# Kernel optimization log

Measured on AMD Instinct MI355X. Metric: run time of the kernel, lower is better.

Reference implementation:

```python
import jax, jax.numpy as jnp
import numpy as np

H = W = 256
L = H * W                      # number of graph vertices / tree leaves
N_NODES = 2 * L - 1            # binary partition tree node count
LAM = 1.0                      # lambda_ (soft-area temperature)


def _grid_edges():
    """4-adjacency grid graph edges (same structure as higra get_4_adjacency_graph)."""
    idx = np.arange(L, dtype=np.int64).reshape(H, W)
    src = np.concatenate([idx[:, :-1].ravel(), idx[:-1, :].ravel()])
    dst = np.concatenate([idx[:, 1:].ravel(), idx[1:, :].ravel()])
    return src.astype(np.int32), dst.astype(np.int32)


def setup_inputs() -> dict:
    key = jax.random.key(0)
    src, dst = _grid_edges()
    ew = jax.random.uniform(key, (src.shape[0],), dtype=jnp.float32)
    return {"edge_weights": ew,
            "edges_src": jnp.asarray(src),
            "edges_dst": jnp.asarray(dst)}


def _build_tree(ew, src, dst):
    """higra.bpt_canonical: Kruskal over stably-sorted edges, building a binary
    merge tree. Leaves are 0..L-1, internal node L+i is created by the i-th MST
    edge. Returns (sizes, mst_edge_map, ancestor paths). All integer structure
    is piecewise-constant w.r.t. edge_weights (no gradient flows through it)."""
    order = np.argsort(ew, kind="stable")
    uf = np.arange(L)

    def find(x):
        r = x
        while uf[r] != r:
            r = uf[r]
        while uf[x] != r:
            uf[x], x = r, uf[x]
        return r

    canon = np.arange(L)                      # tree node of each union-find root
    parent = np.arange(N_NODES)               # self-parent until set (root keeps self)
    sizes = np.ones(N_NODES, dtype=np.float32)
    edge_map = np.zeros(L - 1, dtype=np.int64)
    node = L
    for ei in order:
        a = find(src[ei]); b = find(dst[ei])
        if a == b:
            continue
        na, nb = canon[a], canon[b]
        parent[na] = node
        parent[nb] = node
        sizes[node] = sizes[na] + sizes[nb]
        edge_map[node - L] = ei
        uf[a] = b
        canon[b] = node
        node += 1
    # self-inclusive ancestor paths, padded by repeating the root
    cur = np.arange(N_NODES)
    cols = [cur.copy()]
    while np.any(parent[cur] != cur):
        cur = parent[cur]
        cols.append(cur.copy())
    paths = np.stack(cols, axis=1)            # [N_NODES, D+1]
    return sizes, edge_map, paths


def _softarea(edge_weights, edge_map, sizes_np, paths_np):
    """Soft area of every tree node n:
       area(n) = sum_x sigmoid((alt(n) - d(x, n)) / lambda)
    where d(x,n) is the min ultrametric distance from leaf x to the leaves of n:
      - x in subtree(n), x != n : d = alt(parent(x))
      - x == n (leaf)           : d = 0
      - x outside subtree(n)    : d = alt(lowest ancestor of n containing x).
    Outside leaves are grouped per ancestor a (count = size(a) - size(previous
    node on the path)), giving an O(N * depth) vectorized computation."""
    alt = jnp.concatenate([jnp.zeros((L,), edge_weights.dtype),
                           edge_weights[edge_map]])          # [N_NODES]
    alt_path = alt[paths_np]                                  # [N, D+1]
    size_path = sizes_np[paths_np]                            # constant, numpy
    diff = jnp.asarray(size_path[:, 1:] - size_path[:, :-1])  # 0 on root padding
    outside = jnp.sum(
        diff * jax.nn.sigmoid((alt[:, None] - alt_path[:, 1:]) / LAM), axis=1)

    # inside: each leaf x contributes sigmoid((alt(a_k) - alt(parent(x)))/lam)
    # to every proper ancestor a_k, plus sigmoid(0)=0.5 to itself (alt(leaf)=0).
    lp = paths_np[:L]                                         # [L, D+1]
    alt_lp = alt_path[:L]
    valid = jnp.asarray((lp[:, 1:] != lp[:, :-1]).astype(np.float32))
    vals = jax.nn.sigmoid((alt_lp[:, 1:] - alt_lp[:, 1:2]) / LAM) * valid
    inside = jax.ops.segment_sum(vals.reshape(-1),
                                 jnp.asarray(lp[:, 1:].reshape(-1)),
                                 num_segments=N_NODES)
    inside = inside.at[:L].add(0.5)
    return inside + outside


def reference(edge_weights, edges_src, edges_dst):
    sizes, edge_map, paths = _build_tree(np.asarray(edge_weights),
                                         np.asarray(edges_src),
                                         np.asarray(edges_dst))
    return _softarea(edge_weights, jnp.asarray(edge_map), sizes, paths)
```

## Files before the change

### kernel.cpp

```cpp
#include <hip/hip_runtime.h>
#include <stdint.h>

typedef unsigned int u32;
typedef unsigned short u16;

#define L_VERTS 65536
#define N_EDGES 130560
#define N_NODES 131071
#define NODEPAD 131072

#define CCH 170
#define SCH 768
#define MAXSV 1536
#define HSZ 2048

#define NB 255
#define TPB 64
#define IPT 8
#define IPB 512

__global__ void init_keys(const float* __restrict__ w, u32* __restrict__ keys, u32* __restrict__ vals){
  int i = blockIdx.x*blockDim.x + threadIdx.x;
  if(i < N_EDGES){ keys[i] = __float_as_uint(w[i]); vals[i] = (u32)i; }
}

__global__ void radix_hist(const u32* __restrict__ idx, const u32* __restrict__ keys,
                           u32* __restrict__ histG, int shift){
  __shared__ u32 h[256];
  for(int i=threadIdx.x;i<256;i+=TPB) h[i]=0;
  __syncthreads();
  int base = blockIdx.x*IPB + threadIdx.x*IPT;
  #pragma unroll
  for(int i=0;i<IPT;i++){
    u32 e = idx[base+i];
    u32 d = (keys[e]>>shift)&255u;
    atomicAdd(&h[d],1u);
  }
  __syncthreads();
  for(int i=threadIdx.x;i<256;i+=TPB) histG[i*NB+blockIdx.x]=h[i];
}

__global__ void radix_scan(u32* histG){
  const int M = 256*NB;
  __shared__ u32 sums[1024];
  int t=threadIdx.x; int s=t*64; u32 acc=0;
  for(int i=0;i<64;i++){int id=s+i; if(id<M) acc+=histG[id];}
  sums[t]=acc; __syncthreads();
  for(int off=1; off<1024; off<<=1){
    u32 v=(t>=off)?sums[t-off]:0u;
    __syncthreads();
    sums[t]+=v;
    __syncthreads();
  }
  u32 run = (t==0)?0u:sums[t-1];
  for(int i=0;i<64;i++){int id=s+i; if(id<M){u32 v=histG[id]; histG[id]=run; run+=v;}}
}

__global__ void radix_scatter(const u32* __restrict__ idxIn, const u32* __restrict__ keys,
                              u32* __restrict__ idxOut, const u32* __restrict__ histG, int shift){
  __shared__ u16 thoff[256][TPB];
  int t=threadIdx.x;
  for(int d=t;d<256;d+=TPB) for(int j=0;j<TPB;j++) thoff[d][j]=0;
  __syncthreads();
  int base = blockIdx.x*IPB + t*IPT;
  u32 myv[IPT]; u32 myd[IPT];
  #pragma unroll
  for(int i=0;i<IPT;i++){
    myv[i]=idxIn[base+i];
    myd[i]=(keys[myv[i]]>>shift)&255u;
    thoff[myd[i]][t]++;
  }
  __syncthreads();
  for(int dd=0;dd<4;dd++){
    int d=t*4+dd; u32 run=0;
    for(int j=0;j<TPB;j++){ u32 v=thoff[d][j]; thoff[d][j]=(u16)run; run+=v; }
  }
  __syncthreads();
  #pragma unroll
  for(int i=0;i<IPT;i++){
    u32 d=myd[i];
    u32 pos = histG[d*NB+blockIdx.x] + (u32)thoff[d][t];
    thoff[d][t]++;
    idxOut[pos]=myv[i];
  }
}

__global__ void build_epair(const u32* __restrict__ order, const int* __restrict__ srcv,
                            const int* __restrict__ dstv, u32* __restrict__ epair){
  int p=blockIdx.x*blockDim.x+threadIdx.x;
  if(p>=N_EDGES) return;
  u32 e=order[p];
  epair[p]=((u32)dstv[e]<<16)|(u32)srcv[e];
}

__global__ void init_all(u32* szG,u16* canonTop16,u32* parent,float* alt){
  int i=blockIdx.x*blockDim.x+threadIdx.x;
  if(i<N_NODES){ parent[i]=(u32)i; alt[i]=0.f; }
  if(i<L_VERTS){ szG[i]=1u; canonTop16[i]=0xFFFFu; }
}

__device__ __forceinline__ u32 ald(u32* p){
  return __hip_atomic_load(p, __ATOMIC_RELAXED, __HIP_MEMORY_SCOPE_AGENT);
}
__device__ __forceinline__ void ast(u32* p, u32 v){
  __hip_atomic_store(p, v, __ATOMIC_RELAXED, __HIP_MEMORY_SCOPE_AGENT);
}

__global__ void __launch_bounds__(1024,1) p1_checkpoints(
    const u32* __restrict__ epair,
    u32* szG, u16* lid16, u16* svroot16, u16* svsize16, u16* svnext16, u32* mG)
{
  __shared__ u16 ufL[L_VERTS];
  __shared__ u32 hkey[HSZ];
  __shared__ u32 sufL[MAXSV];
  __shared__ u32 compsz[MAXSV];
  __shared__ u32 repkey[MAXSV];
  __shared__ u32 mcnt;
  u16* hval=(u16*)repkey;
  int t = threadIdx.x;
  for(int i=t;i<L_VERTS/2;i+=1024) ((u32*)ufL)[i]=((2u*(u32)i+1u)<<16)|(2u*(u32)i);
  for(int k=0;k<CCH;k++){
    for(int i=t;i<HSZ;i+=1024) hkey[i]=0xFFFFFFFFu;
    if(t==0) mcnt=0u;
    __syncthreads();
    int base = k*SCH;
    int myslot[2]; int mycnt=0;
    for(int i=t;i<2*SCH;i+=1024){
      u32 pr = epair[base+(i>>1)];
      u32 v = (i&1)? (pr>>16) : (pr&0xFFFFu);
      u32 x=v;
      while(true){ u32 px=ufL[x]; if(px==x)break; u32 g=ufL[px]; if(g!=px) ufL[x]=(u16)g; x=g; }
      u32 r=x;
      if(v!=r) ufL[v]=(u16)r;
      u32 h=(r*2654435761u)>>21;
      int slot;
      while(true){
        u32 old=atomicCAS(&hkey[h],0xFFFFFFFFu,r);
        if(old==0xFFFFFFFFu){
          slot=(int)h;
          u32 id=atomicAdd(&mcnt,1u);
          hval[h]=(u16)id;
          u32 sz=ald(&szG[r]);
          svroot16[k*MAXSV+id]=(u16)r;
          svsize16[k*MAXSV+id]=(u16)(sz-1u);
          break;
        }
        if(old==r){slot=(int)h;break;}
        h=(h+1)&(HSZ-1u);
      }
      myslot[mycnt++]=slot;
    }
    __syncthreads();
    {
      int c=0;
      for(int i=t;i<2*SCH;i+=1024){ lid16[2*base+i]=hval[myslot[c]]; c++; }
    }
    u32 mc=mcnt;
    if(t==0) mG[k]=mc;
    __syncthreads();
    for(u32 s=t;s<mc;s+=1024){ sufL[s]=s; compsz[s]=0u; repkey[s]=0u; }
    __syncthreads();
    for(int i=t;i<SCH;i+=1024){
      u32 lw=((u32*)lid16)[base+i];
      u32 sa=lw&0xFFFFu, sb=lw>>16;
      if(sa==sb) continue;
      while(true){
        u32 x=sa; while(true){u32 p2=sufL[x]; if(p2==x)break; u32 g=sufL[p2]; if(g!=p2) sufL[x]=g; x=g;}
        u32 y=sb; while(true){u32 p2=sufL[y]; if(p2==y)break; u32 g=sufL[p2]; if(g!=p2) sufL[y]=g; y=g;}
        if(x==y) break;
        u32 hi=x>y?x:y, lo=x^y^hi;
        if(atomicCAS(&sufL[hi],hi,lo)==hi) break;
        sa=hi; sb=lo;
      }
    }
    __syncthreads();
    for(u32 s=t;s<mc;s+=1024){
      u32 x=s; while(true){u32 p2=sufL[x]; if(p2==x)break; x=p2;}
      sufL[s]=x;
      u32 sz=(u32)svsize16[k*MAXSV+s]+1u;
      atomicAdd(&compsz[x], sz);
      atomicMax(&repkey[x], (sz<<11) | (2047u-s));
    }
    __syncthreads();
    for(u32 s=t;s<mc;s+=1024){
      u32 rs=sufL[s];
      u32 rep=2047u-(repkey[rs]&2047u);
      u32 wv=(u32)svroot16[k*MAXSV+rep];
      svnext16[k*MAXSV+s]=(u16)wv;
      u32 myroot=(u32)svroot16[k*MAXSV+s];
      if(myroot!=wv) ufL[myroot]=(u16)wv;
      if(s==rep)     ast(&szG[wv], compsz[rs]);
    }
    __syncthreads();
  }
}

__global__ void __launch_bounds__(64) p2_chunk(
  const u16* __restrict__ lid16,
  const u16* __restrict__ svsize16, const u16* __restrict__ svnext16, const u32* __restrict__ mG,
  u16* __restrict__ outChA, u16* __restrict__ outChB, u16* __restrict__ outSize16, u16* __restrict__ outJ16,
  u32* __restrict__ accCnt, u16* __restrict__ compR16, u16* __restrict__ compTop16, u32* __restrict__ ncomp)
{
  int k = blockIdx.x; int t = threadIdx.x;
  __shared__ u16 uf[MAXSV];
  __shared__ u32 csize[MAXSV];
  __shared__ u16 ctop[MAXSV];
  __shared__ u16 svnl[MAXSV];
  __shared__ u32 cmp_s;
  u32 m = mG[k];
  for(u32 s=t;s<m;s+=64){
    uf[s]=(u16)s;
    csize[s]=(u32)svsize16[k*MAXSV+s]+1u;
    ctop[s]=(u16)s;
    svnl[s]=svnext16[k*MAXSV+s];
  }
  if(t==0) cmp_s=0u;
  __syncthreads();
  if(t==0){
    int base=k*SCH;
    u32 cnt=0;
    for(int j=0;j<SCH;j++){
      u32 lw = ((const u32*)lid16)[base+j];
      u32 la = lw & 0xFFFFu, lb = lw >> 16;
      u32 x=la; while(true){u32 px=uf[x]; if(px==x)break; u32 g=uf[px]; uf[x]=(u16)g; x=g;}
      u32 y=lb; while(true){u32 py=uf[y]; if(py==y)break; u32 g=uf[py]; uf[y]=(u16)g; y=g;}
      if(x==y) continue;
      u32 sa=csize[x], sb=csize[y], ns=sa+sb;
      outChA[base+cnt]=ctop[x];
      outChB[base+cnt]=ctop[y];
      outSize16[base+cnt]=(u16)(ns-1u);
      outJ16[base+cnt]=(u16)j;
      u32 win=(sa>=sb)?x:y, los=x^y^win;
      uf[los]=(u16)win; csize[win]=ns; ctop[win]=(u16)(0x8000u|cnt);
      cnt++;
    }
    accCnt[k]=cnt;
  }
  __syncthreads();
  for(u32 s=t;s<m;s+=64){
    if(uf[s]==(u16)s && (ctop[s]&0x8000u)){
      u32 pos=atomicAdd(&cmp_s,1u);
      compR16[k*MAXSV+pos]=svnl[s];
      compTop16[k*MAXSV+pos]=(u16)(ctop[s]&0x7FFFu);
    }
  }
  __syncthreads();
  if(t==0) ncomp[k]=cmp_s;
}

__global__ void __launch_bounds__(1024) p3_stitch(
  const u32* __restrict__ accCnt, const u16* __restrict__ outChA, const u16* __restrict__ outChB,
  const u16* __restrict__ outSize16, const u16* __restrict__ outJ16,
  const u16* __restrict__ svroot16,
  const u16* __restrict__ compR16, const u16* __restrict__ compTop16, const u32* __restrict__ ncomp,
  const u32* __restrict__ order, const float* __restrict__ w,
  u16* __restrict__ canonTop16, u32* __restrict__ parent, float* __restrict__ alt, u16* __restrict__ usize16,
  u32* __restrict__ diag)
{
  __shared__ u32 accBase[CCH];
  int t=threadIdx.x;
  if(t==0){ u32 r=0; for(int k=0;k<CCH;k++){ accBase[k]=r; r+=accCnt[k]; } diag[1]=r; }
  __syncthreads();
  for(int idx=t; idx<N_EDGES; idx+=1024){
    int k = idx/SCH; int j = idx - k*SCH;
    if(j < (int)accCnt[k]){
      u32 nid = (u32)L_VERTS + accBase[k] + (u32)j;
      u32 p = (u32)(k*SCH) + (u32)outJ16[idx];
      alt[nid] = w[order[p]];
      usize16[nid] = outSize16[idx];
      u32 cA=outChA[idx]; if(cA & 0x8000u) parent[(u32)L_VERTS+accBase[k]+(cA&0x7FFFu)] = nid;
      u32 cB=outChB[idx]; if(cB & 0x8000u) parent[(u32)L_VERTS+accBase[k]+(cB&0x7FFFu)] = nid;
    }
  }
  __syncthreads();
  for(int k=0;k<CCH;k++){
    u32 ac=accCnt[k];
    for(u32 j=t;j<ac;j+=1024){
      u32 idx=(u32)(k*SCH)+j;
      u32 nid=(u32)L_VERTS+accBase[k]+j;
      u32 cA=outChA[idx];
      if(!(cA&0x8000u)){
        u32 root=(u32)svroot16[k*MAXSV+cA];
        u32 ct=(u32)canonTop16[root];
        parent[(ct==0xFFFFu)?root:((u32)L_VERTS+ct)]=nid;
      }
      u32 cB=outChB[idx];
      if(!(cB&0x8000u)){
        u32 root=(u32)svroot16[k*MAXSV+cB];
        u32 ct=(u32)canonTop16[root];
        parent[(ct==0xFFFFu)?root:((u32)L_VERTS+ct)]=nid;
      }
    }
    __syncthreads();
    u32 nc=ncomp[k];
    for(u32 j=t;j<nc;j+=1024){
      canonTop16[(u32)compR16[k*MAXSV+j]] = (u16)(accBase[k]+compTop16[k*MAXSV+j]);
    }
    __syncthreads();
  }
}

__global__ void verify_zero(u32* chsum, u32* diag){
  int i=blockIdx.x*blockDim.x+threadIdx.x;
  if(i<L_VERTS) chsum[i]=0u;
  if(i==0){ diag[0]=0u; diag[2]=0u; }
}
__global__ void verify_pass1(const u32* __restrict__ parent, const float* __restrict__ alt,
                             const u16* __restrict__ usize16, u32* chsum, u32* diag){
  int i=blockIdx.x*blockDim.x+threadIdx.x;
  if(i>=N_NODES) return;
  u32 p=parent[i];
  if(p==(u32)i){ atomicAdd(&diag[2],1u); return; }
  u32 sz = (i<L_VERTS)?1u:((u32)usize16[i]+1u);
  atomicAdd(&chsum[p-L_VERTS], sz + (1u<<24));
  if(alt[p] < alt[i]) atomicOr(&diag[0], 4u);
}
__global__ void verify_pass2(const u16* __restrict__ usize16, u32* chsum, u32* diag){
  int i=blockIdx.x*blockDim.x+threadIdx.x;
  if(i==0){
    if(diag[1]!=(u32)(L_VERTS-1)) atomicOr(&diag[0],1u);
    if(diag[2]!=1u)               atomicOr(&diag[0],2u);
  }
  if(i<L_VERTS-1){
    u32 n=(u32)L_VERTS+(u32)i;
    u32 expect=((u32)usize16[n]+1u)+(2u<<24);
    if(chsum[i]!=expect) atomicOr(&diag[0],8u);
  }
  if(i<L_VERTS) chsum[i]=0u;
}
__global__ void fixup(const u32* diag, float* out){
  u32 f=diag[0];
  if(f==0u) return;
  float v = (f&1u)?2.0e6f : (f&2u)?3.0e6f : (f&4u)?4.0e6f : 5.0e6f;
  int i=blockIdx.x*blockDim.x+threadIdx.x;
  if(i<N_NODES) out[i]=v;
}

__device__ __forceinline__ void hvals3(float v, int j0, float* o){
  float v2=v*v, v3=v2*v, v4=v2*v2, v5=v4*v;
  if(j0==0){
    o[0]=0.5f-0.25f*v+v3*(1.f/48.f)-v5*(1.f/480.f);
    o[1]=0.25f-v2*(1.f/16.f)+v4*(1.f/96.f);
    o[2]=v*(1.f/16.f)-v3*(1.f/48.f);
  }else{
    o[0]=v2*(1.f/48.f)-(1.f/48.f);
    o[1]=-v*(1.f/96.f);
    o[2]=(1.f/480.f);
  }
}

__global__ void prep_init(const u32* __restrict__ parent, const u16* __restrict__ usize16,
                          u32* cc, u32* J0, uint2* A0, float* out){
  int n=blockIdx.x*blockDim.x+threadIdx.x;
  if(n>=N_NODES) return;
  out[n] = (n<L_VERTS)?0.5f:0.0f;
  if(n==N_NODES-1){ J0[n]=(u32)n; A0[n]=make_uint2(0u,0u); return; }
  u32 p=parent[n];
  u32 ord=atomicAdd(&cc[p-L_VERTS],1u);
  u32 szP=(u32)usize16[p]+1u;
  u32 szN=(n<L_VERTS)?1u:((u32)usize16[n]+1u);
  u32 sib=szP-szN;
  A0[n]=make_uint2(ord? sib:0u, 1u + (ord? (2u*sib-1u):0u));
  J0[n]=p;
}

__global__ void double_round2(const u32* __restrict__ Jin, const uint2* __restrict__ Ain,
                              u32* __restrict__ Jout, uint2* __restrict__ Aout){
  int n=blockIdx.x*blockDim.x+threadIdx.x;
  if(n>=N_NODES) return;
  u32 j=Jin[n];
  u32 j2=Jin[j];
  u32 j3=Jin[j2];
  uint2 a=Ain[n], aj=Ain[j], b=Ain[j2], bj=Ain[j3];
  Aout[n]=make_uint2(a.x+aj.x+b.x+bj.x, a.y+aj.y+b.y+bj.y);
  Jout[n]=Jin[j3];
}

__global__ void zero_nodeM(float* nodeM){
  int i=blockIdx.x*blockDim.x+threadIdx.x;
  if(i<3*NODEPAD) nodeM[i]=0.f;
}

__global__ void leaf_scatter(const u32* __restrict__ parent, const float* __restrict__ alt,
                             const uint2* __restrict__ accF, float* __restrict__ leafM, int j0){
  int x=blockIdx.x*blockDim.x+threadIdx.x;
  if(x>=L_VERTS) return;
  float b=alt[parent[x]];
  float h[3]; hvals3(b,j0,h);
  u32 pos=accF[x].x;
  leafM[0*L_VERTS+pos]=h[0];
  leafM[1*L_VERTS+pos]=h[1];
  leafM[2*L_VERTS+pos]=h[2];
}

__global__ void node_scatter(const u32* __restrict__ parent, const float* __restrict__ alt,
                             const u16* __restrict__ usize16, const uint2* __restrict__ accF,
                             float* __restrict__ nodeM, int j0){
  int n=blockIdx.x*blockDim.x+threadIdx.x;
  if(n>=N_NODES-1) return;
  u32 p=parent[n];
  u32 szP=(u32)usize16[p]+1u;
  u32 szN=(n<L_VERTS)?1u:((u32)usize16[n]+1u);
  float d=(float)(szP-szN);
  float h[3]; hvals3(alt[p],j0,h);
  u32 q0=accF[n].y;
  u32 q1=q0 + 2u*szN - 1u;
  #pragma unroll
  for(int j=0;j<3;j++){
    float tm=d*h[j];
    atomicAdd(&nodeM[j*NODEPAD+q0], tm);
    atomicAdd(&nodeM[j*NODEPAD+q1], -tm);
  }
}

__global__ void scanA(float* M, u32 slen, float* bsum){
  int j=blockIdx.y; int b=blockIdx.x; int t=threadIdx.x;
  float* arr = M + (size_t)j*slen;
  __shared__ float s[256];
  u32 base=(u32)b*1024u + (u32)t*4u;
  float v0=arr[base],v1=arr[base+1],v2=arr[base+2],v3=arr[base+3];
  v1+=v0; v2+=v1; v3+=v2;
  s[t]=v3; __syncthreads();
  for(int o=1;o<256;o<<=1){ float x=(t>=o)?s[t-o]:0.f; __syncthreads(); s[t]+=x; __syncthreads(); }
  float pre=(t>0)?s[t-1]:0.f;
  arr[base]=v0+pre; arr[base+1]=v1+pre; arr[base+2]=v2+pre; arr[base+3]=v3+pre;
  if(t==255) bsum[j*gridDim.x+b]=s[255];
}

__global__ void scanB(float* bsumL, float* bsumN){
  int t=threadIdx.x;
  if(t<3){ float r=0; for(int i=0;i<64;i++){ float v=bsumL[t*64+i]; bsumL[t*64+i]=r; r+=v; } }
  else if(t<6){ int j=t-3; float r=0; for(int i=0;i<128;i++){ float v=bsumN[j*128+i]; bsumN[j*128+i]=r; r+=v; } }
}

__global__ void inside_eval(const uint2* __restrict__ accF, const float* __restrict__ alt,
                            const u16* __restrict__ usize16, const float* __restrict__ leafM,
                            const float* __restrict__ bsumL, float* __restrict__ out, int j0){
  int a=L_VERTS + blockIdx.x*blockDim.x+threadIdx.x;
  if(a>=N_NODES) return;
  u32 lo=accF[a].x;
  u32 hi=lo + (u32)usize16[a] + 1u;
  float u=alt[a];
  float up=1.f; for(int i=0;i<j0;i++) up*=u;
  float acc=0.f;
  #pragma unroll
  for(int j=0;j<3;j++){
    const float* arr=leafM + (size_t)j*L_VERTS;
    const float* bs=bsumL + j*64;
    float Ph = arr[hi-1u] + bs[(hi-1u)>>10];
    float Pl = lo ? (arr[lo-1u] + bs[(lo-1u)>>10]) : 0.f;
    acc += up*(Ph-Pl);
    up*=u;
  }
  out[a]+=acc;
}

__global__ void outside_eval(const uint2* __restrict__ accF, const float* __restrict__ alt,
                             const float* __restrict__ nodeM, const float* __restrict__ bsumN,
                             float* __restrict__ out, int j0){
  int n=blockIdx.x*blockDim.x+threadIdx.x;
  if(n>=N_NODES) return;
  u32 q=accF[n].y;
  float u=alt[n];
  float up=1.f; for(int i=0;i<j0;i++) up*=u;
  float acc=0.f;
  #pragma unroll
  for(int j=0;j<3;j++){
    float T = nodeM[(size_t)j*NODEPAD+q] + bsumN[j*128 + (q>>10)];
    acc += up*T;
    up*=u;
  }
  out[n]+=acc;
}

__global__ void ws_too_small(float* out){
  int i=blockIdx.x*blockDim.x+threadIdx.x;
  if(i<N_NODES) out[i]=1.0e6f;
}

extern "C" void kernel_launch(void* const* d_in, const int* in_sizes, int n_in,
                              void* d_out, int out_size, void* d_ws, size_t ws_size,
                              hipStream_t stream){
  (void)in_sizes; (void)n_in; (void)out_size;
  const float* w  = (const float*)d_in[0];
  const int* src  = (const int*)d_in[1];
  const int* dst  = (const int*)d_in[2];
  float* out = (float*)d_out;

  char* ws = (char*)d_ws;
  size_t off=0;
  auto alloc=[&](size_t bytes)->void*{ void* p = ws+off; off += (bytes+511)&~(size_t)511; return p; };
  u32* parent   =(u32*)alloc((size_t)N_NODES*4);
  float* alt    =(float*)alloc((size_t)N_NODES*4);
  u16* usize16  =(u16*)alloc((size_t)N_NODES*2);
  u32* diag     =(u32*)alloc(512);
  float* bsumL  =(float*)alloc(3*64*4);
  float* bsumN  =(float*)alloc(3*128*4);
  size_t scratch0=off;
  u32* keys0    =(u32*)alloc((size_t)N_EDGES*4);
  u32* vals0    =(u32*)alloc((size_t)N_EDGES*4);
  u32* vals1    =(u32*)alloc((size_t)N_EDGES*4);
  u32* histG    =(u32*)alloc(256*NB*4);
  u16* canonTop16=(u16*)alloc((size_t)L_VERTS*2);
  u16* outJ16   =(u16*)alloc((size_t)N_EDGES*2);
  u16* svroot16 =(u16*)alloc((size_t)CCH*MAXSV*2);
  u16* svsize16 =(u16*)alloc((size_t)CCH*MAXSV*2);
  u16* svnext16 =(u16*)alloc((size_t)CCH*MAXSV*2);
  u32* mG       =(u32*)alloc(CCH*4);
  u32* accCnt   =(u32*)alloc(CCH*4);
  u32* ncomp    =(u32*)alloc(CCH*4);
  size_t endA=off;
  off=scratch0;
  u32* ccChsum  =(u32*)alloc((size_t)L_VERTS*4);
  u32* J0       =(u32*)alloc((size_t)N_NODES*4);
  u32* J1       =(u32*)alloc((size_t)N_NODES*4);
  uint2* A0     =(uint2*)alloc((size_t)N_NODES*8);
  uint2* A1     =(uint2*)alloc((size_t)N_NODES*8);
  float* leafM  =(float*)alloc((size_t)3*L_VERTS*4);
  float* nodeM  =(float*)alloc((size_t)3*NODEPAD*4);
  size_t endB=off;

  if((endA>ws_size)||(endB>ws_size)){
    ws_too_small<<<(N_NODES+255)/256,256,0,stream>>>(out);
    return;
  }

  u16* lid16    =(u16*)vals1;
  u32* epair    =keys0;
  u16* outChA16 =(u16*)histG;
  u16* outChB16 =(u16*)keys0;
  u16* outSize16=(u16*)((char*)keys0 + (size_t)N_EDGES*2);
  u16* compR16  =svsize16;
  u16* compTop16=svnext16;
  u32* chsum    =ccChsum;
  u32* szG      =(u32*)usize16;

  init_keys<<<(N_EDGES+255)/256,256,0,stream>>>(w,keys0,vals0);
  for(int pass=0;pass<4;pass++){
    const u32* iv = (pass&1)?vals1:vals0;
    u32* ov = (pass&1)?vals0:vals1;
    int shift=pass*8;
    radix_hist   <<<NB,TPB,0,stream>>>(iv,keys0,histG,shift);
    radix_scan   <<<1,1024,0,stream>>>(histG);
    radix_scatter<<<NB,TPB,0,stream>>>(iv,keys0,ov,histG,shift);
  }
  build_epair<<<(N_EDGES+255)/256,256,0,stream>>>(vals0,src,dst,epair);
  init_all<<<(N_NODES+255)/256,256,0,stream>>>(szG,canonTop16,parent,alt);
  p1_checkpoints<<<1,1024,0,stream>>>(epair,szG,lid16,svroot16,svsize16,svnext16,mG);
  p2_chunk<<<CCH,64,0,stream>>>(lid16,svsize16,svnext16,mG,
                                outChA16,outChB16,outSize16,outJ16,accCnt,compR16,compTop16,ncomp);
  p3_stitch<<<1,1024,0,stream>>>(accCnt,outChA16,outChB16,outSize16,outJ16,svroot16,
                                 compR16,compTop16,ncomp,vals0,w,canonTop16,parent,alt,usize16,diag);
  verify_zero <<<(L_VERTS+255)/256,256,0,stream>>>(chsum,diag);
  verify_pass1<<<(N_NODES+255)/256,256,0,stream>>>(parent,alt,usize16,chsum,diag);
  verify_pass2<<<(L_VERTS+255)/256,256,0,stream>>>(usize16,chsum,diag);
  prep_init<<<(N_NODES+255)/256,256,0,stream>>>(parent,usize16,ccChsum,J0,A0,out);
  for(int r=0;r<9;r++){
    if((r&1)==0) double_round2<<<(N_NODES+255)/256,256,0,stream>>>(J0,A0,J1,A1);
    else         double_round2<<<(N_NODES+255)/256,256,0,stream>>>(J1,A1,J0,A0);
  }
  const uint2* accF=A1;
  for(int j0=0;j0<=3;j0+=3){
    zero_nodeM<<<(3*NODEPAD+255)/256,256,0,stream>>>(nodeM);
    leaf_scatter<<<(L_VERTS+255)/256,256,0,stream>>>(parent,alt,accF,leafM,j0);
    node_scatter<<<(N_NODES+255)/256,256,0,stream>>>(parent,alt,usize16,accF,nodeM,j0);
    scanA<<<dim3(64,3),256,0,stream>>>(leafM,L_VERTS,bsumL);
    scanA<<<dim3(128,3),256,0,stream>>>(nodeM,NODEPAD,bsumN);
    scanB<<<1,64,0,stream>>>(bsumL,bsumN);
    inside_eval<<<(L_VERTS+255)/256,256,0,stream>>>(accF,alt,usize16,leafM,bsumL,out,j0);
    outside_eval<<<(N_NODES+255)/256,256,0,stream>>>(accF,alt,nodeM,bsumN,out,j0);
  }
  fixup<<<(N_NODES+255)/256,256,0,stream>>>(diag,out);
}
```

Measured before the change: 3.215 ms.

## Drop tree verification passes and fuse scatter, scan and eval kernels

Removes the verification kernels (verify_zero/pass1/pass2/fixup) and their diag bookkeeping, replacing them with a small zero kernel for the count buffer. Merges leaf and node scatter into one kernel, the two scan launches into one grid, and inside/outside evaluation into one kernel, so each j0 iteration launches fewer kernels. In p1, hval gets its own shared array so the per-chunk init can move before the first barrier, and the global szG size loads move out of the hash-insert loop into a separate pass. The output is no longer overwritten with sentinel values if the tree build is wrong.

```diff
diff --git a/kernel.cpp b/kernel.cpp
--- a/kernel.cpp
+++ b/kernel.cpp
@@ -112,15 +112,16 @@
 {
   __shared__ u16 ufL[L_VERTS];
   __shared__ u32 hkey[HSZ];
+  __shared__ u16 hval[HSZ];
   __shared__ u32 sufL[MAXSV];
   __shared__ u32 compsz[MAXSV];
   __shared__ u32 repkey[MAXSV];
   __shared__ u32 mcnt;
-  u16* hval=(u16*)repkey;
   int t = threadIdx.x;
   for(int i=t;i<L_VERTS/2;i+=1024) ((u32*)ufL)[i]=((2u*(u32)i+1u)<<16)|(2u*(u32)i);
   for(int k=0;k<CCH;k++){
     for(int i=t;i<HSZ;i+=1024) hkey[i]=0xFFFFFFFFu;
+    for(u32 s=t;s<MAXSV;s+=1024){ sufL[s]=s; compsz[s]=0u; repkey[s]=0u; }
     if(t==0) mcnt=0u;
     __syncthreads();
     int base = k*SCH;
@@ -140,9 +141,7 @@
           slot=(int)h;
           u32 id=atomicAdd(&mcnt,1u);
           hval[h]=(u16)id;
-          u32 sz=ald(&szG[r]);
           svroot16[k*MAXSV+id]=(u16)r;
-          svsize16[k*MAXSV+id]=(u16)(sz-1u);
           break;
         }
         if(old==r){slot=(int)h;break;}
@@ -151,14 +150,16 @@
       myslot[mycnt++]=slot;
     }
     __syncthreads();
+    u32 mc=mcnt;
+    if(t==0) mG[k]=mc;
+    for(u32 s=t;s<mc;s+=1024){
+      u32 r=(u32)svroot16[k*MAXSV+s];
+      svsize16[k*MAXSV+s]=(u16)(ald(&szG[r])-1u);
+    }
     {
       int c=0;
       for(int i=t;i<2*SCH;i+=1024){ lid16[2*base+i]=hval[myslot[c]]; c++; }
     }
-    u32 mc=mcnt;
-    if(t==0) mG[k]=mc;
-    __syncthreads();
-    for(u32 s=t;s<mc;s+=1024){ sufL[s]=s; compsz[s]=0u; repkey[s]=0u; }
     __syncthreads();
     for(int i=t;i<SCH;i+=1024){
       u32 lw=((u32*)lid16)[base+i];
@@ -254,12 +255,11 @@
   const u16* __restrict__ svroot16,
   const u16* __restrict__ compR16, const u16* __restrict__ compTop16, const u32* __restrict__ ncomp,
   const u32* __restrict__ order, const float* __restrict__ w,
-  u16* __restrict__ canonTop16, u32* __restrict__ parent, float* __restrict__ alt, u16* __restrict__ usize16,
-  u32* __restrict__ diag)
+  u16* __restrict__ canonTop16, u32* __restrict__ parent, float* __restrict__ alt, u16* __restrict__ usize16)
 {
   __shared__ u32 accBase[CCH];
   int t=threadIdx.x;
-  if(t==0){ u32 r=0; for(int k=0;k<CCH;k++){ accBase[k]=r; r+=accCnt[k]; } diag[1]=r; }
+  if(t==0){ u32 r=0; for(int k=0;k<CCH;k++){ accBase[k]=r; r+=accCnt[k]; } }
   __syncthreads();
   for(int idx=t; idx<N_EDGES; idx+=1024){
     int k = idx/SCH; int j = idx - k*SCH;
@@ -300,42 +300,6 @@
   }
 }
 
-__global__ void verify_zero(u32* chsum, u32* diag){
-  int i=blockIdx.x*blockDim.x+threadIdx.x;
-  if(i<L_VERTS) chsum[i]=0u;
-  if(i==0){ diag[0]=0u; diag[2]=0u; }
-}
-__global__ void verify_pass1(const u32* __restrict__ parent, const float* __restrict__ alt,
-                             const u16* __restrict__ usize16, u32* chsum, u32* diag){
-  int i=blockIdx.x*blockDim.x+threadIdx.x;
-  if(i>=N_NODES) return;
-  u32 p=parent[i];
-  if(p==(u32)i){ atomicAdd(&diag[2],1u); return; }
-  u32 sz = (i<L_VERTS)?1u:((u32)usize16[i]+1u);
-  atomicAdd(&chsum[p-L_VERTS], sz + (1u<<24));
-  if(alt[p] < alt[i]) atomicOr(&diag[0], 4u);
-}
-__global__ void verify_pass2(const u16* __restrict__ usize16, u32* chsum, u32* diag){
-  int i=blockIdx.x*blockDim.x+threadIdx.x;
-  if(i==0){
-    if(diag[1]!=(u32)(L_VERTS-1)) atomicOr(&diag[0],1u);
-    if(diag[2]!=1u)               atomicOr(&diag[0],2u);
-  }
-  if(i<L_VERTS-1){
-    u32 n=(u32)L_VERTS+(u32)i;
-    u32 expect=((u32)usize16[n]+1u)+(2u<<24);
-    if(chsum[i]!=expect) atomicOr(&diag[0],8u);
-  }
-  if(i<L_VERTS) chsum[i]=0u;
-}
-__global__ void fixup(const u32* diag, float* out){
-  u32 f=diag[0];
-  if(f==0u) return;
-  float v = (f&1u)?2.0e6f : (f&2u)?3.0e6f : (f&4u)?4.0e6f : 5.0e6f;
-  int i=blockIdx.x*blockDim.x+threadIdx.x;
-  if(i<N_NODES) out[i]=v;
-}
-
 __device__ __forceinline__ void hvals3(float v, int j0, float* o){
   float v2=v*v, v3=v2*v, v4=v2*v2, v5=v4*v;
   if(j0==0){
@@ -347,6 +311,11 @@
     o[1]=-v*(1.f/96.f);
     o[2]=(1.f/480.f);
   }
+}
+
+__global__ void zero_cc(u32* cc){
+  int i=blockIdx.x*blockDim.x+threadIdx.x;
+  if(i<L_VERTS) cc[i]=0u;
 }
 
 __global__ void prep_init(const u32* __restrict__ parent, const u16* __restrict__ usize16,
@@ -381,50 +350,50 @@
   if(i<3*NODEPAD) nodeM[i]=0.f;
 }
 
-__global__ void leaf_scatter(const u32* __restrict__ parent, const float* __restrict__ alt,
-                             const uint2* __restrict__ accF, float* __restrict__ leafM, int j0){
-  int x=blockIdx.x*blockDim.x+threadIdx.x;
-  if(x>=L_VERTS) return;
-  float b=alt[parent[x]];
-  float h[3]; hvals3(b,j0,h);
-  u32 pos=accF[x].x;
-  leafM[0*L_VERTS+pos]=h[0];
-  leafM[1*L_VERTS+pos]=h[1];
-  leafM[2*L_VERTS+pos]=h[2];
-}
-
-__global__ void node_scatter(const u32* __restrict__ parent, const float* __restrict__ alt,
-                             const u16* __restrict__ usize16, const uint2* __restrict__ accF,
-                             float* __restrict__ nodeM, int j0){
+__global__ void scatter_all(const u32* __restrict__ parent, const float* __restrict__ alt,
+                            const u16* __restrict__ usize16, const uint2* __restrict__ accF,
+                            float* __restrict__ leafM, float* __restrict__ nodeM, int j0){
   int n=blockIdx.x*blockDim.x+threadIdx.x;
-  if(n>=N_NODES-1) return;
+  if(n>=N_NODES) return;
   u32 p=parent[n];
-  u32 szP=(u32)usize16[p]+1u;
-  u32 szN=(n<L_VERTS)?1u:((u32)usize16[n]+1u);
-  float d=(float)(szP-szN);
   float h[3]; hvals3(alt[p],j0,h);
-  u32 q0=accF[n].y;
-  u32 q1=q0 + 2u*szN - 1u;
-  #pragma unroll
-  for(int j=0;j<3;j++){
-    float tm=d*h[j];
-    atomicAdd(&nodeM[j*NODEPAD+q0], tm);
-    atomicAdd(&nodeM[j*NODEPAD+q1], -tm);
-  }
-}
-
-__global__ void scanA(float* M, u32 slen, float* bsum){
-  int j=blockIdx.y; int b=blockIdx.x; int t=threadIdx.x;
-  float* arr = M + (size_t)j*slen;
+  uint2 af=accF[n];
+  if(n<L_VERTS){
+    u32 pos=af.x;
+    leafM[0*L_VERTS+pos]=h[0];
+    leafM[1*L_VERTS+pos]=h[1];
+    leafM[2*L_VERTS+pos]=h[2];
+  }
+  if(n<N_NODES-1){
+    u32 szP=(u32)usize16[p]+1u;
+    u32 szN=(n<L_VERTS)?1u:((u32)usize16[n]+1u);
+    float d=(float)(szP-szN);
+    u32 q0=af.y;
+    u32 q1=q0 + 2u*szN - 1u;
+    #pragma unroll
+    for(int j=0;j<3;j++){
+      float tm=d*h[j];
+      atomicAdd(&nodeM[j*NODEPAD+q0], tm);
+      atomicAdd(&nodeM[j*NODEPAD+q1], -tm);
+    }
+  }
+}
+
+__global__ void scanAll(float* __restrict__ leafM, float* __restrict__ nodeM,
+                        float* __restrict__ bsumL, float* __restrict__ bsumN){
+  int b=blockIdx.x; int t=threadIdx.x;
+  float* arr; u32 base; float* bs;
+  if(b<3*64){ int row=b>>6, blk=b&63;  arr=leafM+(size_t)row*L_VERTS;  base=(u32)blk*1024u; bs=&bsumL[row*64+blk]; }
+  else      { int bb=b-192; int row=bb>>7, blk=bb&127; arr=nodeM+(size_t)row*NODEPAD; base=(u32)blk*1024u; bs=&bsumN[row*128+blk]; }
   __shared__ float s[256];
-  u32 base=(u32)b*1024u + (u32)t*4u;
+  base += (u32)t*4u;
   float v0=arr[base],v1=arr[base+1],v2=arr[base+2],v3=arr[base+3];
   v1+=v0; v2+=v1; v3+=v2;
   s[t]=v3; __syncthreads();
   for(int o=1;o<256;o<<=1){ float x=(t>=o)?s[t-o]:0.f; __syncthreads(); s[t]+=x; __syncthreads(); }
   float pre=(t>0)?s[t-1]:0.f;
   arr[base]=v0+pre; arr[base+1]=v1+pre; arr[base+2]=v2+pre; arr[base+3]=v3+pre;
-  if(t==255) bsum[j*gridDim.x+b]=s[255];
+  if(t==255) *bs=s[255];
 }
 
 __global__ void scanB(float* bsumL, float* bsumN){
@@ -433,42 +402,36 @@
   else if(t<6){ int j=t-3; float r=0; for(int i=0;i<128;i++){ float v=bsumN[j*128+i]; bsumN[j*128+i]=r; r+=v; } }
 }
 
-__global__ void inside_eval(const uint2* __restrict__ accF, const float* __restrict__ alt,
-                            const u16* __restrict__ usize16, const float* __restrict__ leafM,
-                            const float* __restrict__ bsumL, float* __restrict__ out, int j0){
-  int a=L_VERTS + blockIdx.x*blockDim.x+threadIdx.x;
-  if(a>=N_NODES) return;
-  u32 lo=accF[a].x;
-  u32 hi=lo + (u32)usize16[a] + 1u;
-  float u=alt[a];
-  float up=1.f; for(int i=0;i<j0;i++) up*=u;
-  float acc=0.f;
-  #pragma unroll
-  for(int j=0;j<3;j++){
-    const float* arr=leafM + (size_t)j*L_VERTS;
-    const float* bs=bsumL + j*64;
-    float Ph = arr[hi-1u] + bs[(hi-1u)>>10];
-    float Pl = lo ? (arr[lo-1u] + bs[(lo-1u)>>10]) : 0.f;
-    acc += up*(Ph-Pl);
-    up*=u;
-  }
-  out[a]+=acc;
-}
-
-__global__ void outside_eval(const uint2* __restrict__ accF, const float* __restrict__ alt,
-                             const float* __restrict__ nodeM, const float* __restrict__ bsumN,
-                             float* __restrict__ out, int j0){
+__global__ void eval_all(const uint2* __restrict__ accF, const float* __restrict__ alt,
+                         const u16* __restrict__ usize16, const float* __restrict__ leafM,
+                         const float* __restrict__ nodeM, const float* __restrict__ bsumL,
+                         const float* __restrict__ bsumN, float* __restrict__ out, int j0){
   int n=blockIdx.x*blockDim.x+threadIdx.x;
   if(n>=N_NODES) return;
-  u32 q=accF[n].y;
+  uint2 af=accF[n];
   float u=alt[n];
-  float up=1.f; for(int i=0;i<j0;i++) up*=u;
-  float acc=0.f;
+  float up0=1.f; for(int i=0;i<j0;i++) up0*=u;
+  u32 q=af.y;
+  float acc=0.f, up=up0;
   #pragma unroll
   for(int j=0;j<3;j++){
     float T = nodeM[(size_t)j*NODEPAD+q] + bsumN[j*128 + (q>>10)];
     acc += up*T;
     up*=u;
+  }
+  if(n>=L_VERTS){
+    u32 lo=af.x;
+    u32 hi=lo + (u32)usize16[n] + 1u;
+    up=up0;
+    #pragma unroll
+    for(int j=0;j<3;j++){
+      const float* arr=leafM + (size_t)j*L_VERTS;
+      const float* bs=bsumL + j*64;
+      float Ph = arr[hi-1u] + bs[(hi-1u)>>10];
+      float Pl = lo ? (arr[lo-1u] + bs[(lo-1u)>>10]) : 0.f;
+      acc += up*(Ph-Pl);
+      up*=u;
+    }
   }
   out[n]+=acc;
 }
@@ -493,7 +456,6 @@
   u32* parent   =(u32*)alloc((size_t)N_NODES*4);
   float* alt    =(float*)alloc((size_t)N_NODES*4);
   u16* usize16  =(u16*)alloc((size_t)N_NODES*2);
-  u32* diag     =(u32*)alloc(512);
   float* bsumL  =(float*)alloc(3*64*4);
   float* bsumN  =(float*)alloc(3*128*4);
   size_t scratch0=off;
@@ -532,7 +494,6 @@
   u16* outSize16=(u16*)((char*)keys0 + (size_t)N_EDGES*2);
   u16* compR16  =svsize16;
   u16* compTop16=svnext16;
-  u32* chsum    =ccChsum;
   u32* szG      =(u32*)usize16;
 
   init_keys<<<(N_EDGES+255)/256,256,0,stream>>>(w,keys0,vals0);
@@ -550,10 +511,8 @@
   p2_chunk<<<CCH,64,0,stream>>>(lid16,svsize16,svnext16,mG,
                                 outChA16,outChB16,outSize16,outJ16,accCnt,compR16,compTop16,ncomp);
   p3_stitch<<<1,1024,0,stream>>>(accCnt,outChA16,outChB16,outSize16,outJ16,svroot16,
-                                 compR16,compTop16,ncomp,vals0,w,canonTop16,parent,alt,usize16,diag);
-  verify_zero <<<(L_VERTS+255)/256,256,0,stream>>>(chsum,diag);
-  verify_pass1<<<(N_NODES+255)/256,256,0,stream>>>(parent,alt,usize16,chsum,diag);
-  verify_pass2<<<(L_VERTS+255)/256,256,0,stream>>>(usize16,chsum,diag);
+                                 compR16,compTop16,ncomp,vals0,w,canonTop16,parent,alt,usize16);
+  zero_cc<<<(L_VERTS+255)/256,256,0,stream>>>(ccChsum);
   prep_init<<<(N_NODES+255)/256,256,0,stream>>>(parent,usize16,ccChsum,J0,A0,out);
   for(int r=0;r<9;r++){
     if((r&1)==0) double_round2<<<(N_NODES+255)/256,256,0,stream>>>(J0,A0,J1,A1);
@@ -562,13 +521,9 @@
   const uint2* accF=A1;
   for(int j0=0;j0<=3;j0+=3){
     zero_nodeM<<<(3*NODEPAD+255)/256,256,0,stream>>>(nodeM);
-    leaf_scatter<<<(L_VERTS+255)/256,256,0,stream>>>(parent,alt,accF,leafM,j0);
-    node_scatter<<<(N_NODES+255)/256,256,0,stream>>>(parent,alt,usize16,accF,nodeM,j0);
-    scanA<<<dim3(64,3),256,0,stream>>>(leafM,L_VERTS,bsumL);
-    scanA<<<dim3(128,3),256,0,stream>>>(nodeM,NODEPAD,bsumN);
+    scatter_all<<<(N_NODES+255)/256,256,0,stream>>>(parent,alt,usize16,accF,leafM,nodeM,j0);
+    scanAll<<<576,256,0,stream>>>(leafM,nodeM,bsumL,bsumN);
     scanB<<<1,64,0,stream>>>(bsumL,bsumN);
-    inside_eval<<<(L_VERTS+255)/256,256,0,stream>>>(accF,alt,usize16,leafM,bsumL,out,j0);
-    outside_eval<<<(N_NODES+255)/256,256,0,stream>>>(accF,alt,nodeM,bsumN,out,j0);
-  }
-  fixup<<<(N_NODES+255)/256,256,0,stream>>>(diag,out);
-}
+    eval_all<<<(N_NODES+255)/256,256,0,stream>>>(accF,alt,usize16,leafM,nodeM,bsumL,bsumN,out,j0);
+  }
+}
```

Result: faster. 2.988 ms (-7.0%).
